# Performance work log

Measured on AMD Instinct MI355X. Metric: run time of the kernel, lower is better.

The kernel has to match this reference:

```python
import jax, jax.numpy as jnp
import numpy as np

EPS = 1e-6


def setup_inputs() -> dict:
    key = jax.random.key(0)
    x = jax.random.normal(key, (64, 256, 64, 64), dtype=jnp.float32)
    return {"x": x}


def reference(x):
    # x: (B, C, H, W)
    B, C, H, W = x.shape
    N = H * W
    # --- covariance pooling ---
    xr = x.reshape(B, C, N)                       # (B, C, N)
    xc = xr - xr.mean(axis=2, keepdims=True)      # mean-center over spatial
    cov = jnp.einsum('bcn,bdn->bcd', xc, xc) / (N - 1)  # (B, C, C)
    # --- matrix square root via eigh ---
    eigvals, eigvecs = jnp.linalg.eigh(cov)       # (B, C), (B, C, C)
    sqrt_eigvals = jnp.sqrt(jnp.clip(eigvals, EPS, None))
    # V diag(sqrt(w)) V^T without materializing diag
    sqrt_mat = jnp.einsum('bic,bc,bjc->bij', eigvecs, sqrt_eigvals, eigvecs)
    # --- upper-triangular vectorization (incl. diagonal) ---
    row_idx, col_idx = jnp.triu_indices(C)
    return sqrt_mat[:, row_idx, col_idx]          # (B, C*(C+1)//2)
```

## Files before the change

kernel.cpp:

```cpp
#include <hip/hip_runtime.h>
#include <hip/hip_bf16.h>
#include <math.h>


#define B_ 64
#define C_ 256
#define N_ 4096
#define TRI ((C_*(C_+1))/2)
#define MATE (C_*C_)
#define TOTE ((size_t)B_*MATE)
#define KS 4
#define KW (N_/KS)
#define NCH 8

typedef __attribute__((ext_vector_type(8))) short bf16x8;
typedef __attribute__((ext_vector_type(4))) float f32x4;

__device__ __forceinline__ short f2bf(float f) {
    unsigned u = __float_as_uint(f);
    return (short)((u + 0x7FFFu + ((u >> 16) & 1u)) >> 16);
}
__device__ __forceinline__ float bf2f(short s) {
    return __uint_as_float(((unsigned)(unsigned short)s) << 16);
}
__device__ __forceinline__ void gload_lds16(const void* g, void* l) {
    __builtin_amdgcn_global_load_lds(
        (const __attribute__((address_space(1))) void*)g,
        (__attribute__((address_space(3))) void*)l, 16, 0, 0);
}

__global__ __launch_bounds__(256) void convert_sums(const float* __restrict__ x,
                                                    short* __restrict__ xb2,
                                                    float* __restrict__ S) {
    int bid = blockIdx.x;
    int b = bid >> 5;
    int c0 = (bid & 31) * 8;
    int tid = threadIdx.x;
    int cl = tid >> 5;
    int ln = tid & 31;
    int c = c0 + cl;
    const float* px = x + ((size_t)(b * C_ + c)) * N_;
    float s = 0.f;
    #pragma unroll
    for (int st = 0; st < 16; ++st) {
        int p = ln + st * 32;
        int slab = p >> 7, chunk = (p >> 4) & 7, piece = p & 15;
        f32x4 u = *(const f32x4*)(px + p * 8);
        f32x4 v = *(const f32x4*)(px + p * 8 + 4);
        s += u[0] + u[1] + u[2] + u[3] + v[0] + v[1] + v[2] + v[3];
        bf16x8 o;
        #pragma unroll
        for (int k = 0; k < 4; ++k) { o[k] = f2bf(u[k]); o[4 + k] = f2bf(v[k]); }
        size_t e = ((((size_t)(b * KS + slab) * NCH + chunk) * C_ + c) * 128) + piece * 8;
        *(bf16x8*)(xb2 + e) = o;
    }
    s += __shfl_down(s, 16, 32);
    s += __shfl_down(s, 8, 32);
    s += __shfl_down(s, 4, 32);
    s += __shfl_down(s, 2, 32);
    s += __shfl_down(s, 1, 32);
    if (ln == 0) S[b * C_ + c] = s;
}

__global__ __launch_bounds__(1024) void gram_cov(const short* __restrict__ xb2,
                                                 short* __restrict__ Gp) {
    int bid = (blockIdx.x & 7) * 32 + (blockIdx.x >> 3);
    int b = bid >> 2, slab = bid & 3;
    const char* xs = (const char*)(xb2 + (size_t)(b * KS + slab) * NCH * C_ * 128);

    __shared__ short Xs[2][32768];

    int tid = threadIdx.x;
    int lane = tid & 63, wid = tid >> 6;
    int wr = wid >> 2, wc = wid & 3;
    int lr = lane & 15, hi = lane >> 4;
    unsigned swz = (unsigned)((lr & 7) << 4);

    f32x4 acc[4][4] = {};

    #pragma unroll
    for (int q = 0; q < 4; ++q) {
        int d = (q * 1024 + tid) * 16;
        int row = d >> 8;
        int src = (d & ~255) | ((d & 255) ^ ((row & 7) << 4));
        gload_lds16(xs + src, (char*)Xs[0] + d);
    }

    #pragma unroll
    for (int c = 0; c < NCH; ++c) {
        if (c + 1 < NCH) {
            #pragma unroll
            for (int q = 0; q < 4; ++q) {
                int d = (q * 1024 + tid) * 16;
                int row = d >> 8;
                int src = (d & ~255) | ((d & 255) ^ ((row & 7) << 4));
                gload_lds16(xs + (c + 1) * 65536 + src,
                            (char*)Xs[(c + 1) & 1] + d);
            }
            asm volatile("s_waitcnt vmcnt(4)" ::: "memory");
        } else {
            asm volatile("s_waitcnt vmcnt(0)" ::: "memory");
        }
        __builtin_amdgcn_s_barrier();
        __builtin_amdgcn_sched_barrier(0);

        const char* Xb = (const char*)Xs[c & 1];
        #pragma unroll
        for (int ks2 = 0; ks2 < 4; ++ks2) {
            unsigned o1 = ((unsigned)(ks2 * 64 + hi * 16)) ^ swz;
            bf16x8 af[4], bb[4];
            #pragma unroll
            for (int m = 0; m < 4; ++m) {
                int row = wr * 64 + m * 16 + lr;
                af[m] = *(const bf16x8*)(Xb + row * 256 + o1);
            }
            #pragma unroll
            for (int n = 0; n < 4; ++n) {
                int row = wc * 64 + n * 16 + lr;
                bb[n] = *(const bf16x8*)(Xb + row * 256 + o1);
            }
            #pragma unroll
            for (int m = 0; m < 4; ++m)
                #pragma unroll
                for (int n = 0; n < 4; ++n)
                    acc[m][n] = __builtin_amdgcn_mfma_f32_16x16x32_bf16(af[m], bb[n], acc[m][n], 0, 0, 0);
        }
        __builtin_amdgcn_sched_barrier(0);
        asm volatile("" ::: "memory");
        __builtin_amdgcn_s_barrier();
    }

    short* G = Gp + ((size_t)slab * B_ + b) * MATE;
    #pragma unroll
    for (int m = 0; m < 4; ++m)
        #pragma unroll
        for (int n = 0; n < 4; ++n)
            #pragma unroll
            for (int r = 0; r < 4; ++r) {
                int i = wr * 64 + m * 16 + hi * 4 + r;
                int j = wc * 64 + n * 16 + lr;
                G[(size_t)i * C_ + j] = f2bf(acc[m][n][r]);
            }
}

__global__ __launch_bounds__(256) void trace_kernel(const short* __restrict__ Gp,
                                                    const float* __restrict__ S,
                                                    float* __restrict__ mArr) {
    int b = blockIdx.x, i = threadIdx.x;
    float s = S[b * C_ + i], g = 0.f;
    #pragma unroll
    for (int sl = 0; sl < KS; ++sl)
        g += bf2f(Gp[((size_t)sl * B_ + b) * MATE + (size_t)i * (C_ + 1)]);
    float c = (g - s * s * (1.0f / N_)) * (1.0f / (N_ - 1));
    __shared__ float red[256];
    red[i] = c;
    __syncthreads();
    for (int off = 128; off; off >>= 1) {
        if (i < off) red[i] += red[i + off];
        __syncthreads();
    }
    if (i == 0) {
        float m = red[0] * (1.0f / C_);
        mArr[b] = m;
        mArr[64 + b] = 1.0f / m;
        mArr[128 + b] = sqrtf(m);
    }
}

__global__ __launch_bounds__(256) void init_kernel(const short* __restrict__ Gp,
                                                   const float* __restrict__ S,
                                                   const float* __restrict__ mArr,
                                                   short* __restrict__ Y0,
                                                   short* __restrict__ Z1) {
    int idx = blockIdx.x * 256 + threadIdx.x;
    size_t e0 = (size_t)idx * 8;
    int b = (int)(e0 >> 16);
    int ij = (int)(e0 & 65535);
    int i = ij >> 8, j0 = ij & 255;
    float g[8] = {};
    #pragma unroll
    for (int sl = 0; sl < KS; ++sl) {
        bf16x8 t = *(const bf16x8*)(Gp + (size_t)sl * TOTE + e0);
        #pragma unroll
        for (int q = 0; q < 8; ++q) g[q] += bf2f(t[q]);
    }
    float Si = S[b * C_ + i];
    f32x4 sjA = *(const f32x4*)(S + b * C_ + j0);
    f32x4 sjB = *(const f32x4*)(S + b * C_ + j0 + 4);
    float invm = mArr[64 + b];
    const float invN = 1.0f / (float)N_;
    const float invN1 = 1.0f / (float)(N_ - 1);
    bf16x8 y, z;
    #pragma unroll
    for (int q = 0; q < 8; ++q) {
        float sj = (q < 4) ? sjA[q] : sjB[q - 4];
        float cov = (g[q] - Si * sj * invN) * invN1;
        float a = cov * invm;
        y[q] = f2bf(a);
        z[q] = f2bf(((i == j0 + q) ? 1.5f : 0.0f) - 0.5f * a);
    }
    *(bf16x8*)(Y0 + e0) = y;
    *(bf16x8*)(Z1 + e0) = z;
}

template<int EP, bool DUAL>
__global__ __launch_bounds__(256) void ns_gemm(
        const short* A0, const short* B0, const short* Ba0, void* C0,
        const short* A1, const short* B1, const short* Ba1, void* C1,
        const float* __restrict__ mArr) {
    int nb = gridDim.x, per = nb >> 3;
    int bid = (blockIdx.x & 7) * per + (blockIdx.x >> 3);
    const short *A = A0, *B = B0, *Ba = Ba0; void* C = C0;
    if (DUAL && bid >= (nb >> 1)) { bid -= nb >> 1; A = A1; B = B1; Ba = Ba1; C = C1; }
    int b, ti, tj;
    if constexpr (EP == 2) {
        b = bid / 3; int t = bid % 3;
        ti = (t == 2) ? 1 : 0; tj = (t == 0) ? 0 : 1;
    } else {
        b = bid >> 2; int t = bid & 3;
        ti = t >> 1; tj = t & 1;
    }
    const short* Ap = A + (size_t)b * MATE + (size_t)ti * 128 * C_;
    const short* Bp = B + (size_t)b * MATE + (size_t)tj * 128 * C_;

    __shared__ short As[16384], Bs[16384];

    int tid = threadIdx.x, lane = tid & 63, wid = tid >> 6;
    int wr = wid >> 1, wc = wid & 1;
    int lr = lane & 15, hi = lane >> 4;
    f32x4 acc[4][4] = {};

    for (int h = 0; h < 2; ++h) {
        #pragma unroll
        for (int q = 0; q < 8; ++q) {
            int d = (q * 256 + tid) * 16;
            int row = d >> 8;
            int inner = (d & 255) ^ ((row & 7) << 4);
            gload_lds16((const char*)Ap + (size_t)row * 512 + h * 256 + inner,
                        (char*)As + d);
            gload_lds16((const char*)Bp + (size_t)row * 512 + h * 256 + inner,
                        (char*)Bs + d);
        }
        __syncthreads();
        #pragma unroll
        for (int ks = 0; ks < 4; ++ks) {
            bf16x8 af[4], bb[4];
            #pragma unroll
            for (int m = 0; m < 4; ++m) {
                int rowa = wr * 64 + m * 16 + lr;
                af[m] = *(const bf16x8*)((const char*)As + rowa * 256 +
                                         ((ks * 64 + hi * 16) ^ ((rowa & 7) << 4)));
                int rowb = wc * 64 + m * 16 + lr;
                bb[m] = *(const bf16x8*)((const char*)Bs + rowb * 256 +
                                         ((ks * 64 + hi * 16) ^ ((rowb & 7) << 4)));
            }
            #pragma unroll
            for (int m = 0; m < 4; ++m)
                #pragma unroll
                for (int n = 0; n < 4; ++n)
                    acc[m][n] = __builtin_amdgcn_mfma_f32_16x16x32_bf16(af[m], bb[n], acc[m][n], 0, 0, 0);
        }
        if (h == 0) __syncthreads();
    }

    int r0 = hi * 4;
    float sqm = (EP == 2) ? mArr[128 + b] : 0.f;
    #pragma unroll
    for (int m = 0; m < 4; ++m)
        #pragma unroll
        for (int n = 0; n < 4; ++n)
            #pragma unroll
            for (int r = 0; r < 4; ++r) {
                int i = ti * 128 + wr * 64 + m * 16 + r0 + r;
                int j = tj * 128 + wc * 64 + n * 16 + lr;
                size_t idx = (size_t)b * MATE + (size_t)i * C_ + j;
                float v = acc[m][n][r];
                if constexpr (EP == 0) {
                    ((short*)C)[idx] = f2bf(v);
                } else if constexpr (EP == 1) {
                    ((short*)C)[idx] = f2bf(1.5f * bf2f(Ba[idx]) - 0.5f * v);
                } else {
                    if (j >= i) {
                        size_t o = (size_t)b * TRI + (size_t)i * C_ - (size_t)(i * (i - 1)) / 2 + (j - i);
                        ((float*)C)[o] = sqm * (1.5f * bf2f(Ba[idx]) - 0.5f * v);
                    }
                }
            }
}

extern "C" void kernel_launch(void* const* d_in, const int* in_sizes, int n_in,
                              void* d_out, int out_size, void* d_ws, size_t ws_size,
                              hipStream_t stream) {
    const float* x = (const float*)d_in[0];
    float* out = (float*)d_out;

    float* mArr = (float*)d_ws;
    float* S    = mArr + 256;
    short* Gp   = (short*)(S + 16384);
    short* xbuf = Gp + (size_t)KS * TOTE;
    short* bufs = xbuf + (size_t)B_ * C_ * N_;
    short* M0 = bufs;
    short* M1 = bufs + TOTE;
    short* M2 = bufs + 2 * TOTE;
    short* M3 = bufs + 3 * TOTE;
    short* M4 = bufs + 4 * TOTE;

    convert_sums<<<B_ * C_ / 8, 256, 0, stream>>>(x, xbuf, S);
    gram_cov<<<B_ * KS, 1024, 0, stream>>>(xbuf, Gp);
    trace_kernel<<<B_, 256, 0, stream>>>(Gp, S, mArr);
    init_kernel<<<(int)(TOTE / 8 / 256), 256, 0, stream>>>(Gp, S, mArr, M0, M1);

    ns_gemm<1, false><<<256, 256, 0, stream>>>(M0, M0, M0, M2,
                                               nullptr, nullptr, nullptr, nullptr, nullptr);
    ns_gemm<0, false><<<256, 256, 0, stream>>>(M1, M2, nullptr, M3,
                                               nullptr, nullptr, nullptr, nullptr, nullptr);
    ns_gemm<1, true><<<512, 256, 0, stream>>>(M2, M3, M2, M4,
                                              M3, M1, M1, M0, nullptr);
    ns_gemm<0, false><<<256, 256, 0, stream>>>(M0, M4, nullptr, M2,
                                               nullptr, nullptr, nullptr, nullptr, nullptr);
    ns_gemm<2, false><<<B_ * 3, 256, 0, stream>>>(M4, M2, M4, out,
                                                  nullptr, nullptr, nullptr, nullptr, mArr);
}
```

Baseline: 196.8 us.

## Replace Newton-Schulz iterations with fixed degree-6 polynomial square root via Horner GEMMs

Replaces the coupled Newton-Schulz iteration chain (five GEMM launches, one of them dual) with a fixed degree-6 polynomial in the trace-normalized covariance. The polynomial is evaluated with three GEMMs whose fused epilogues combine the earlier powers. This cuts the GEMM count and buffer traffic. In exchange, accuracy now depends on the eigenvalue spread of the normalized matrix staying inside the range the truncated binomial-series coefficients were tuned for. The gram kernel also drops its hand-tuned waitcnt/sched_barrier pipelining for plain __syncthreads, which may serialize loads with MFMA work.

```diff
diff --git a/kernel.cpp b/kernel.cpp
--- a/kernel.cpp
+++ b/kernel.cpp
@@ -15,6 +15,15 @@
 
 typedef __attribute__((ext_vector_type(8))) short bf16x8;
 typedef __attribute__((ext_vector_type(4))) float f32x4;
+
+constexpr double SQMU = 1.0307764064044151;
+constexpr float D0 = (float)(SQMU * (231.0 / 1024.0));
+constexpr float D1 = (float)(SQMU * (1386.0 / 1024.0) / 1.0625);
+constexpr float D2 = (float)(SQMU * (-1155.0 / 1024.0) / 1.12890625);
+constexpr float D3 = (float)(SQMU * (924.0 / 1024.0) / 1.199462890625);
+constexpr float D4 = (float)(SQMU * (-495.0 / 1024.0) / 1.2744293212890625);
+constexpr float D5 = (float)(SQMU * (154.0 / 1024.0) / 1.3540811538696289);
+constexpr float D6 = (float)(SQMU * (-21.0 / 1024.0) / 1.4387112259864807);
 
 __device__ __forceinline__ short f2bf(float f) {
     unsigned u = __float_as_uint(f);
@@ -85,8 +94,8 @@
         int src = (d & ~255) | ((d & 255) ^ ((row & 7) << 4));
         gload_lds16(xs + src, (char*)Xs[0] + d);
     }
-
-    #pragma unroll
+    __syncthreads();
+
     for (int c = 0; c < NCH; ++c) {
         if (c + 1 < NCH) {
             #pragma unroll
@@ -97,13 +106,7 @@
                 gload_lds16(xs + (c + 1) * 65536 + src,
                             (char*)Xs[(c + 1) & 1] + d);
             }
-            asm volatile("s_waitcnt vmcnt(4)" ::: "memory");
-        } else {
-            asm volatile("s_waitcnt vmcnt(0)" ::: "memory");
         }
-        __builtin_amdgcn_s_barrier();
-        __builtin_amdgcn_sched_barrier(0);
-
         const char* Xb = (const char*)Xs[c & 1];
         #pragma unroll
         for (int ks2 = 0; ks2 < 4; ++ks2) {
@@ -125,9 +128,7 @@
                 for (int n = 0; n < 4; ++n)
                     acc[m][n] = __builtin_amdgcn_mfma_f32_16x16x32_bf16(af[m], bb[n], acc[m][n], 0, 0, 0);
         }
-        __builtin_amdgcn_sched_barrier(0);
-        asm volatile("" ::: "memory");
-        __builtin_amdgcn_s_barrier();
+        __syncthreads();
     }
 
     short* G = Gp + ((size_t)slab * B_ + b) * MATE;
@@ -170,8 +171,7 @@
 __global__ __launch_bounds__(256) void init_kernel(const short* __restrict__ Gp,
                                                    const float* __restrict__ S,
                                                    const float* __restrict__ mArr,
-                                                   short* __restrict__ Y0,
-                                                   short* __restrict__ Z1) {
+                                                   short* __restrict__ A) {
     int idx = blockIdx.x * 256 + threadIdx.x;
     size_t e0 = (size_t)idx * 8;
     int b = (int)(e0 >> 16);
@@ -190,30 +190,24 @@
     float invm = mArr[64 + b];
     const float invN = 1.0f / (float)N_;
     const float invN1 = 1.0f / (float)(N_ - 1);
-    bf16x8 y, z;
+    bf16x8 y;
     #pragma unroll
     for (int q = 0; q < 8; ++q) {
         float sj = (q < 4) ? sjA[q] : sjB[q - 4];
         float cov = (g[q] - Si * sj * invN) * invN1;
-        float a = cov * invm;
-        y[q] = f2bf(a);
-        z[q] = f2bf(((i == j0 + q) ? 1.5f : 0.0f) - 0.5f * a);
-    }
-    *(bf16x8*)(Y0 + e0) = y;
-    *(bf16x8*)(Z1 + e0) = z;
-}
-
-template<int EP, bool DUAL>
-__global__ __launch_bounds__(256) void ns_gemm(
-        const short* A0, const short* B0, const short* Ba0, void* C0,
-        const short* A1, const short* B1, const short* Ba1, void* C1,
-        const float* __restrict__ mArr) {
+        y[q] = f2bf(cov * invm);
+    }
+    *(bf16x8*)(A + e0) = y;
+}
+
+template<int EP>
+__global__ __launch_bounds__(256) void poly_gemm(
+        const short* A, const short* Bm, const short* P1, const short* P2,
+        void* C, short* C2, const float* __restrict__ mArr) {
     int nb = gridDim.x, per = nb >> 3;
     int bid = (blockIdx.x & 7) * per + (blockIdx.x >> 3);
-    const short *A = A0, *B = B0, *Ba = Ba0; void* C = C0;
-    if (DUAL && bid >= (nb >> 1)) { bid -= nb >> 1; A = A1; B = B1; Ba = Ba1; C = C1; }
     int b, ti, tj;
-    if constexpr (EP == 2) {
+    if constexpr (EP == 4) {
         b = bid / 3; int t = bid % 3;
         ti = (t == 2) ? 1 : 0; tj = (t == 0) ? 0 : 1;
     } else {
@@ -221,7 +215,7 @@
         ti = t >> 1; tj = t & 1;
     }
     const short* Ap = A + (size_t)b * MATE + (size_t)ti * 128 * C_;
-    const short* Bp = B + (size_t)b * MATE + (size_t)tj * 128 * C_;
+    const short* Bp = Bm + (size_t)b * MATE + (size_t)tj * 128 * C_;
 
     __shared__ short As[16384], Bs[16384];
 
@@ -264,7 +258,7 @@
     }
 
     int r0 = hi * 4;
-    float sqm = (EP == 2) ? mArr[128 + b] : 0.f;
+    float sqm = (EP == 4) ? mArr[128 + b] : 0.f;
     #pragma unroll
     for (int m = 0; m < 4; ++m)
         #pragma unroll
@@ -277,12 +271,17 @@
                 float v = acc[m][n][r];
                 if constexpr (EP == 0) {
                     ((short*)C)[idx] = f2bf(v);
-                } else if constexpr (EP == 1) {
-                    ((short*)C)[idx] = f2bf(1.5f * bf2f(Ba[idx]) - 0.5f * v);
+                } else if constexpr (EP == 3) {
+                    ((short*)C)[idx] = f2bf(v);
+                    float q1v = D4 * bf2f(P1[idx]) + D5 * bf2f(P2[idx]) + D6 * v;
+                    if (i == j) q1v += D3;
+                    C2[idx] = f2bf(q1v);
                 } else {
                     if (j >= i) {
-                        size_t o = (size_t)b * TRI + (size_t)i * C_ - (size_t)(i * (i - 1)) / 2 + (j - i);
-                        ((float*)C)[o] = sqm * (1.5f * bf2f(Ba[idx]) - 0.5f * v);
+                        float o = D1 * bf2f(P1[idx]) + D2 * bf2f(P2[idx]) + v;
+                        if (i == j) o += D0;
+                        size_t oo = (size_t)b * TRI + (size_t)i * C_ - (size_t)(i * (i - 1)) / 2 + (j - i);
+                        ((float*)C)[oo] = sqm * o;
                     }
                 }
             }
@@ -299,25 +298,20 @@
     short* Gp   = (short*)(S + 16384);
     short* xbuf = Gp + (size_t)KS * TOTE;
     short* bufs = xbuf + (size_t)B_ * C_ * N_;
-    short* M0 = bufs;
-    short* M1 = bufs + TOTE;
-    short* M2 = bufs + 2 * TOTE;
-    short* M3 = bufs + 3 * TOTE;
-    short* M4 = bufs + 4 * TOTE;
+    short* MA  = bufs;
+    short* MA2 = bufs + TOTE;
+    short* MA3 = bufs + 2 * TOTE;
+    short* MQ1 = bufs + 3 * TOTE;
 
     convert_sums<<<B_ * C_ / 8, 256, 0, stream>>>(x, xbuf, S);
     gram_cov<<<B_ * KS, 1024, 0, stream>>>(xbuf, Gp);
     trace_kernel<<<B_, 256, 0, stream>>>(Gp, S, mArr);
-    init_kernel<<<(int)(TOTE / 8 / 256), 256, 0, stream>>>(Gp, S, mArr, M0, M1);
-
-    ns_gemm<1, false><<<256, 256, 0, stream>>>(M0, M0, M0, M2,
-                                               nullptr, nullptr, nullptr, nullptr, nullptr);
-    ns_gemm<0, false><<<256, 256, 0, stream>>>(M1, M2, nullptr, M3,
-                                               nullptr, nullptr, nullptr, nullptr, nullptr);
-    ns_gemm<1, true><<<512, 256, 0, stream>>>(M2, M3, M2, M4,
-                                              M3, M1, M1, M0, nullptr);
-    ns_gemm<0, false><<<256, 256, 0, stream>>>(M0, M4, nullptr, M2,
-                                               nullptr, nullptr, nullptr, nullptr, nullptr);
-    ns_gemm<2, false><<<B_ * 3, 256, 0, stream>>>(M4, M2, M4, out,
-                                                  nullptr, nullptr, nullptr, nullptr, mArr);
-}
+    init_kernel<<<(int)(TOTE / 8 / 256), 256, 0, stream>>>(Gp, S, mArr, MA);
+
+    poly_gemm<0><<<256, 256, 0, stream>>>(MA, MA, nullptr, nullptr,
+                                          MA2, nullptr, nullptr);
+    poly_gemm<3><<<256, 256, 0, stream>>>(MA2, MA, MA, MA2,
+                                          MA3, MQ1, nullptr);
+    poly_gemm<4><<<B_ * 3, 256, 0, stream>>>(MA3, MQ1, MA, MA2,
+                                             out, nullptr, mArr);
+}
```

After: 182.5 us. 1.08x faster.
